# Optimization experiments

Measured on AMD Instinct MI355X. Metric: run time of the kernel, lower is better.

The kernel has to match this reference:

```python
import jax, jax.numpy as jnp
import numpy as np

EPS_GN = 1e-8
EPS_ATTN = 1e-8


def setup_inputs() -> dict:
    key = jax.random.key(0)
    ks = jax.random.split(key, 13)
    B, C, N = 4, 512, 2048
    s = 0.02
    return {
        "x": jax.random.normal(ks[0], (B, C, N), jnp.float32),
        "dw_w": jax.random.normal(ks[1], (C, 3), jnp.float32) * s,
        "pw_w": jax.random.normal(ks[2], (C, C), jnp.float32) * s,
        "u_w": jax.random.normal(ks[3], (2 * C, C), jnp.float32) * s,
        "u_b": jax.random.normal(ks[4], (2 * C,), jnp.float32) * s,
        "v_w": jax.random.normal(ks[5], (2 * C, C), jnp.float32) * s,
        "v_b": jax.random.normal(ks[6], (2 * C,), jnp.float32) * s,
        "h_w": jax.random.normal(ks[7], (C, C), jnp.float32) * s,
        "h_b": jax.random.normal(ks[8], (C,), jnp.float32) * s,
        "q_w": jax.random.normal(ks[9], (C, C), jnp.float32) * s,
        "k_w": jax.random.normal(ks[10], (C, C), jnp.float32) * s,
        "o_w": jax.random.normal(ks[11], (C, 2 * C), jnp.float32) * s,
        "o_b": jax.random.normal(ks[12], (C,), jnp.float32) * s,
    }


def reference(x, dw_w, pw_w, u_w, u_b, v_w, v_b, h_w, h_b, q_w, k_w, o_w, o_b):
    # x: [B, C, N]
    C = x.shape[1]
    # GroupNorm(1, C): normalize over (C, N) per sample; affine is identity-init
    # in torch but we follow the module math with default weight=1, bias=0
    mean = jnp.mean(x, axis=(1, 2), keepdims=True)
    var = jnp.var(x, axis=(1, 2), keepdims=True)
    z = (x - mean) * jax.lax.rsqrt(var + EPS_GN)

    # local depthwise conv k=3, pad=1 (cross-correlation), no bias
    zp = jnp.pad(z, ((0, 0), (0, 0), (1, 1)))
    dw = (dw_w[:, 0, None] * zp[:, :, :-2]
          + dw_w[:, 1, None] * zp[:, :, 1:-1]
          + dw_w[:, 2, None] * zp[:, :, 2:])
    # pointwise conv (no bias)
    z = z + jnp.einsum('oc,bcn->bon', pw_w, dw)

    u = jax.nn.sigmoid(jnp.einsum('oc,bcn->bon', u_w, z) + u_b[:, None])  # [B,2C,N]
    v = jnp.einsum('oc,bcn->bon', v_w, z) + v_b[:, None]                  # [B,2C,N]
    h = jnp.einsum('oc,bcn->bno', h_w, z) + h_b                           # [B,N,C]

    q = h @ q_w.T  # [B,N,C]
    k = h @ k_w.T  # [B,N,C]
    scale = 1.0 / jnp.sqrt(jnp.float32(C))

    logits = jnp.einsum('bnc,bmc->bnm', q, k) * scale
    a = jax.nn.relu(logits)
    a = a * a
    a = a / (jnp.sum(a, axis=-1, keepdims=True) + EPS_ATTN)

    av = jnp.einsum('bnm,bom->bon', a, v)  # [B,2C,N]
    y = jnp.einsum('oc,bcn->bon', o_w, u * av) + o_b[:, None]
    return x + y
```

## Files before the change

### kernel.cpp

```cpp
#include <hip/hip_runtime.h>
#include <hip/hip_bf16.h>
#include <cstdint>

typedef __bf16 bhalf;
typedef __bf16 bhalf8 __attribute__((ext_vector_type(8)));
typedef float f32x4 __attribute__((ext_vector_type(4)));

enum { EPI_Z2=0, EPI_BIAS=2, EPI_QK=3, EPI_Y=6, EPI_ST=7 };

__device__ __forceinline__ void gl_lds16(const void* g, void* l) {
  __builtin_amdgcn_global_load_lds(
      (const __attribute__((address_space(1))) unsigned int*)g,
      (__attribute__((address_space(3))) unsigned int*)l,
      16, 0, 0);
}
__device__ __forceinline__ void barrier_raw() { asm volatile("s_barrier" ::: "memory"); }
#define VMW(n)  asm volatile("s_waitcnt vmcnt(" #n ")" ::: "memory")
#define LGKM0() asm volatile("s_waitcnt lgkmcnt(0)" ::: "memory")

__device__ __forceinline__ unsigned char to_fp8(float v){
  return (unsigned char)(__builtin_amdgcn_cvt_pk_fp8_f32(v, v, 0, false) & 0xff);
}


__global__ void __launch_bounds__(256, 2)
gsc8(const unsigned char* __restrict__ Q, const unsigned char* __restrict__ Kp,
     unsigned char* __restrict__ Wsc, float* __restrict__ rden, float scale)
{
  constexpr int DBUF = 256*64;
  __shared__ __align__(16) char lds[3*DBUF];

  const int gx = gridDim.x, gy = gridDim.y;
  const int nwg = gx*gy;
  const int flat = blockIdx.y*gx + blockIdx.x;
  const int q8 = nwg>>3, r8 = nwg&7, xcd = flat&7, o8 = flat>>3;
  const int w = (xcd<r8 ? xcd*(q8+1) : r8*(q8+1)+(xcd-r8)*q8) + o8;
  const int bx = w % gx, by = w / gx;
  const int m0 = by*128, n0 = bx*128;
  const int bz = blockIdx.z;
  const int K = 512;

  const unsigned char* Ab = Q  + (long)bz*2048*512;
  const unsigned char* Bb = Kp + (long)bz*2048*512;

  const int tid = threadIdx.x;
  const int wid = tid>>6, lane = tid&63;
  const int lm = lane&15, kq = lane>>4;
  const int wm = wid>>1, wn = wid&1;
  const int srow = lane>>2;
  const int csw8 = ((lane&3) ^ ((lane>>3)&3))*16;
  int coff[2];
  #pragma unroll
  for (int ksl=0; ksl<2; ksl++)
    coff[ksl] = ((((ksl*2 + (kq>>1)) ^ ((lm>>1)&3)))<<4) + ((kq&1)<<3);

  f32x4 acc[4][4];
  #pragma unroll
  for (int i=0;i<4;i++)
    #pragma unroll
    for (int j=0;j<4;j++) acc[i][j] = f32x4{0.f,0.f,0.f,0.f};

  auto stage = [&](int kt){
    char* base = lds + (kt%3)*DBUF;
    const int k0 = kt*64;
    #pragma unroll
    for (int c=0;c<4;c++){
      const int r0 = c*64 + wid*16;
      char* d = base + r0*64;
      const unsigned char* g = (r0 < 128)
        ? Ab + (long)(m0 + r0 + srow)*K + k0 + csw8
        : Bb + (long)(n0 + r0 - 128 + srow)*K + k0 + csw8;
      gl_lds16(g, d);
    }
  };

  long af[4][2], bf[4][2];
  auto readA = [&](int kt){
    char* base = lds + (kt%3)*DBUF;
    #pragma unroll
    for (int i2=0;i2<4;i2++)
      #pragma unroll
      for (int ksl=0;ksl<2;ksl++)
        af[i2][ksl] = *(const long*)(base + (wm*64 + i2*16 + lm)*64 + coff[ksl]);
  };
  auto readB = [&](int kt, int jh){
    char* base = lds + (kt%3)*DBUF;
    #pragma unroll
    for (int j2=0;j2<2;j2++)
      #pragma unroll
      for (int ksl=0;ksl<2;ksl++)
        bf[jh*2+j2][ksl] = *(const long*)(base + (128 + wn*64 + jh*32 + j2*16 + lm)*64 + coff[ksl]);
  };
  auto mfma16 = [&](int jh){
    __builtin_amdgcn_s_setprio(1);
    #pragma unroll
    for (int i2=0;i2<4;i2++)
      #pragma unroll
      for (int j2=0;j2<2;j2++)
        #pragma unroll
        for (int ksl=0;ksl<2;ksl++)
          acc[i2][jh*2+j2] = __builtin_amdgcn_mfma_f32_16x16x32_fp8_fp8(
              af[i2][ksl], bf[jh*2+j2][ksl], acc[i2][jh*2+j2], 0,0,0);
    __builtin_amdgcn_s_setprio(0);
  };

  const int NT = 8;
  stage(0); stage(1);
  for (int kt=0; kt<NT; ++kt){
    if (kt==NT-1) { VMW(0); } else { VMW(4); }
    barrier_raw();
    readA(kt); readB(kt,0);
    if (kt+2<NT) stage(kt+2);
    mfma16(0);
    readB(kt,1);
    mfma16(1);
  }
  barrier_raw();

  float rs[4][4];
  #pragma unroll
  for (int i=0;i<4;i++)
    #pragma unroll
    for (int r=0;r<4;r++) rs[i][r]=0.f;
  #pragma unroll
  for (int i=0;i<4;i++){
    #pragma unroll
    for (int j=0;j<4;j++){
      const int lcol = wn*64 + j*16 + lm;
      #pragma unroll
      for (int r=0;r<4;r++){
        const int lrow = wm*64 + i*16 + kq*4 + r;
        float v = acc[i][j][r];
        v *= scale; v = fmaxf(v,0.f); v = v*v;
        rs[i][r] += v;
        const int lb = lrow*128 + ((((lcol>>4) ^ (lrow&7)))<<4) + (lcol&15);
        *(unsigned char*)(lds + lb) = to_fp8(v);
      }
    }
  }
  float* rd = rden + (long)bz*2048;
  #pragma unroll
  for (int i=0;i<4;i++){
    const int rbase = m0 + wm*64 + i*16 + kq*4;
    #pragma unroll
    for (int r=0;r<4;r++){
      float s = rs[i][r];
      s += __shfl_xor(s,1); s += __shfl_xor(s,2);
      s += __shfl_xor(s,4); s += __shfl_xor(s,8);
      if (lm==0) atomicAdd(rd + rbase + r, s);
    }
  }
  LGKM0();
  barrier_raw();
  unsigned char* obase = Wsc + (long)bz*2048*2048 + (long)m0*2048 + n0;
  #pragma unroll
  for (int it=0; it<4; ++it){
    const int g = (it*256 + tid)*16;
    const int row = g >> 7, off = g & 127;
    const int lb = row*128 + ((((off>>4) ^ (row&7)))<<4);
    uint4 val = *(const uint4*)(lds + lb);
    *(uint4*)(obase + (long)row*2048 + off) = val;
  }
}

__global__ void __launch_bounds__(256, 2)
guv8(const unsigned char* __restrict__ A, const unsigned char* __restrict__ Bw,
     bhalf* __restrict__ Ub, unsigned char* __restrict__ Vfm,
     const float* __restrict__ ubias, const float* __restrict__ vbias)
{
  constexpr int DBUF = 256*64;
  __shared__ __align__(16) char lds[3*DBUF];

  const int gx = gridDim.x, gy = gridDim.y;
  const int nwg = gx*gy;
  const int flat = blockIdx.y*gx + blockIdx.x;
  const int q8 = nwg>>3, r8 = nwg&7, xcd = flat&7, o8 = flat>>3;
  const int w = (xcd<r8 ? xcd*(q8+1) : r8*(q8+1)+(xcd-r8)*q8) + o8;
  const int bx = w % gx, by = w / gx;
  const int m0 = by*128, n0 = bx*128;
  const int K = 512;

  const int tid = threadIdx.x;
  const int wid = tid>>6, lane = tid&63;
  const int lm = lane&15, kq = lane>>4;
  const int wm = wid>>1, wn = wid&1;
  const int srow = lane>>2;
  const int csw8 = ((lane&3) ^ ((lane>>3)&3))*16;
  int coff[2];
  #pragma unroll
  for (int ksl=0; ksl<2; ksl++)
    coff[ksl] = ((((ksl*2 + (kq>>1)) ^ ((lm>>1)&3)))<<4) + ((kq&1)<<3);

  f32x4 acc[4][4];
  #pragma unroll
  for (int i=0;i<4;i++)
    #pragma unroll
    for (int j=0;j<4;j++) acc[i][j] = f32x4{0.f,0.f,0.f,0.f};

  auto stage = [&](int kt){
    char* base = lds + (kt%3)*DBUF;
    const int k0 = kt*64;
    #pragma unroll
    for (int c=0;c<4;c++){
      const int r0 = c*64 + wid*16;
      char* d = base + r0*64;
      const unsigned char* g = (r0 < 128)
        ? A  + (long)(m0 + r0 + srow)*K + k0 + csw8
        : Bw + (long)(n0 + r0 - 128 + srow)*K + k0 + csw8;
      gl_lds16(g, d);
    }
  };

  long af[4][2], bf[4][2];
  auto readA = [&](int kt){
    char* base = lds + (kt%3)*DBUF;
    #pragma unroll
    for (int i2=0;i2<4;i2++)
      #pragma unroll
      for (int ksl=0;ksl<2;ksl++)
        af[i2][ksl] = *(const long*)(base + (wm*64 + i2*16 + lm)*64 + coff[ksl]);
  };
  auto readB = [&](int kt, int jh){
    char* base = lds + (kt%3)*DBUF;
    #pragma unroll
    for (int j2=0;j2<2;j2++)
      #pragma unroll
      for (int ksl=0;ksl<2;ksl++)
        bf[jh*2+j2][ksl] = *(const long*)(base + (128 + wn*64 + jh*32 + j2*16 + lm)*64 + coff[ksl]);
  };
  auto mfma16 = [&](int jh){
    __builtin_amdgcn_s_setprio(1);
    #pragma unroll
    for (int i2=0;i2<4;i2++)
      #pragma unroll
      for (int j2=0;j2<2;j2++)
        #pragma unroll
        for (int ksl=0;ksl<2;ksl++)
          acc[i2][jh*2+j2] = __builtin_amdgcn_mfma_f32_16x16x32_fp8_fp8(
              af[i2][ksl], bf[jh*2+j2][ksl], acc[i2][jh*2+j2], 0,0,0);
    __builtin_amdgcn_s_setprio(0);
  };

  const int NT = 8;
  stage(0); stage(1);
  for (int kt=0; kt<NT; ++kt){
    if (kt==NT-1) { VMW(0); } else { VMW(4); }
    barrier_raw();
    readA(kt); readB(kt,0);
    if (kt+2<NT) stage(kt+2);
    mfma16(0);
    readB(kt,1);
    mfma16(1);
  }
  barrier_raw();

  const bool uh = n0 < 1024;
  if (uh){
    #pragma unroll
    for (int i=0;i<4;i++){
      #pragma unroll
      for (int j=0;j<4;j++){
        const int lcol = wn*64 + j*16 + lm;
        #pragma unroll
        for (int r=0;r<4;r++){
          const int lrow = wm*64 + i*16 + kq*4 + r;
          float v = acc[i][j][r] + ubias[n0 + lcol];
          v = 1.f/(1.f + __expf(-v));
          const int cb = lcol*2;
          const int lb = lrow*256 + (((cb>>5) ^ ((lrow>>2)&3))<<5) + (cb&31);
          *(bhalf*)(lds + lb) = (bhalf)v;
        }
      }
    }
    LGKM0();
    barrier_raw();
    char* obase = (char*)Ub + 2*((long)m0*1024 + n0);
    #pragma unroll
    for (int it=0; it<8; ++it){
      const int g = (it*256 + tid)*16;
      const int row = g >> 8, off = g & 255;
      const int lb = row*256 + (((off>>5) ^ ((row>>2)&3))<<5) + (off&31);
      uint4 val = *(const uint4*)(lds + lb);
      *(uint4*)(obase + (long)row*2048 + off) = val;
    }
  } else {
    #pragma unroll
    for (int i=0;i<4;i++){
      #pragma unroll
      for (int j=0;j<4;j++){
        const int lcol = wn*64 + j*16 + lm;
        #pragma unroll
        for (int r=0;r<4;r++){
          const int lrow = wm*64 + i*16 + kq*4 + r;
          float v = acc[i][j][r] + vbias[n0 - 1024 + lcol];
          const int lb = lcol*128 + ((((lrow>>4) ^ (lcol&7)))<<4) + (lrow&15);
          *(unsigned char*)(lds + lb) = to_fp8(v);
        }
      }
    }
    LGKM0();
    barrier_raw();
    unsigned char* vb = Vfm + ((long)(m0>>11)*1024*2048 + (long)(n0-1024)*2048 + (m0 & 2047));
    #pragma unroll
    for (int it=0; it<4; ++it){
      const int g = (it*256 + tid)*16;
      const int row = g >> 7, off = g & 127;
      const int lb = row*128 + ((((off>>4) ^ (row&7)))<<4);
      uint4 val = *(const uint4*)(lds + lb);
      *(uint4*)(vb + (long)row*2048 + off) = val;
    }
  }
}

__global__ void __launch_bounds__(256, 2)
g4k8(const unsigned char* __restrict__ A, const unsigned char* __restrict__ Bw,
     bhalf* __restrict__ Out,
     const bhalf* __restrict__ ub, const float* __restrict__ rden,
     int K, long sB, int rowshift)
{
  constexpr int DBUF = 256*64;
  __shared__ __align__(16) char lds[4*DBUF];

  const int gx = gridDim.x, gy = gridDim.y;
  const int nwg = gx*gy;
  const int flat = blockIdx.y*gx + blockIdx.x;
  const int q8 = nwg>>3, r8 = nwg&7, xcd = flat&7, o8 = flat>>3;
  const int w = (xcd<r8 ? xcd*(q8+1) : r8*(q8+1)+(xcd-r8)*q8) + o8;
  const int bx = w % gx, by = w / gx;
  const int m0 = by*128, n0 = bx*128;

  const unsigned char* Bb = Bw + (long)(m0>>rowshift)*sB;

  const int tid = threadIdx.x;
  const int wid = tid>>6, lane = tid&63;
  const int lm = lane&15, kq = lane>>4;
  const int wm = wid>>1, wn = wid&1;
  const int srow = lane>>2;
  const int csw8 = ((lane&3) ^ ((lane>>3)&3))*16;
  int coff[2];
  #pragma unroll
  for (int ksl=0; ksl<2; ksl++)
    coff[ksl] = ((((ksl*2 + (kq>>1)) ^ ((lm>>1)&3)))<<4) + ((kq&1)<<3);

  f32x4 acc[4][4];
  #pragma unroll
  for (int i=0;i<4;i++)
    #pragma unroll
    for (int j=0;j<4;j++) acc[i][j] = f32x4{0.f,0.f,0.f,0.f};

  auto stage = [&](int kt){
    char* base = lds + (kt&3)*DBUF;
    const int k0 = kt*64;
    #pragma unroll
    for (int c=0;c<4;c++){
      const int r0 = c*64 + wid*16;
      char* d = base + r0*64;
      const unsigned char* g = (r0 < 128)
        ? A  + (long)(m0 + r0 + srow)*K + k0 + csw8
        : Bb + (long)(n0 + r0 - 128 + srow)*K + k0 + csw8;
      gl_lds16(g, d);
    }
  };

  long af[4][2], bf[4][2];
  auto readA = [&](int kt){
    char* base = lds + (kt&3)*DBUF;
    #pragma unroll
    for (int i2=0;i2<4;i2++)
      #pragma unroll
      for (int ksl=0;ksl<2;ksl++)
        af[i2][ksl] = *(const long*)(base + (wm*64 + i2*16 + lm)*64 + coff[ksl]);
  };
  auto readB = [&](int kt, int jh){
    char* base = lds + (kt&3)*DBUF;
    #pragma unroll
    for (int j2=0;j2<2;j2++)
      #pragma unroll
      for (int ksl=0;ksl<2;ksl++)
        bf[jh*2+j2][ksl] = *(const long*)(base + (128 + wn*64 + jh*32 + j2*16 + lm)*64 + coff[ksl]);
  };
  auto mfma16 = [&](int jh){
    __builtin_amdgcn_s_setprio(1);
    #pragma unroll
    for (int i2=0;i2<4;i2++)
      #pragma unroll
      for (int j2=0;j2<2;j2++)
        #pragma unroll
        for (int ksl=0;ksl<2;ksl++)
          acc[i2][jh*2+j2] = __builtin_amdgcn_mfma_f32_16x16x32_fp8_fp8(
              af[i2][ksl], bf[jh*2+j2][ksl], acc[i2][jh*2+j2], 0,0,0);
    __builtin_amdgcn_s_setprio(0);
  };

  const int NT = K>>6;
  stage(0); stage(1); stage(2);
  for (int kt=0; kt<NT; ++kt){
    if (kt==NT-1)      { VMW(0); }
    else if (kt==NT-2) { VMW(4); }
    else               { VMW(8); }
    barrier_raw();
    readA(kt); readB(kt,0);
    if (kt+3<NT) stage(kt+3);
    mfma16(0);
    readB(kt,1);
    mfma16(1);
  }
  barrier_raw();

  char* obase = (char*)Out + 2*((long)m0*1024 + n0);
  #pragma unroll
  for (int i=0;i<4;i++){
    #pragma unroll
    for (int j=0;j<4;j++){
      const int lcol = wn*64 + j*16 + lm;
      #pragma unroll
      for (int r=0;r<4;r++){
        const int lrow = wm*64 + i*16 + kq*4 + r;
        const int rowg = m0 + lrow;
        float v = acc[i][j][r];
        float den = rden[rowg];
        v *= __builtin_amdgcn_rcpf(den + 1e-8f);
        v *= (float)ub[(long)rowg*1024 + n0 + lcol];
        const int cb = lcol*2;
        const int lb = lrow*256 + (((cb>>5) ^ ((lrow>>2)&3))<<5) + (cb&31);
        *(bhalf*)(lds + lb) = (bhalf)v;
      }
    }
  }
  LGKM0();
  barrier_raw();
  #pragma unroll
  for (int it=0; it<8; ++it){
    const int g = (it*256 + tid)*16;
    const int row = g >> 8, off = g & 255;
    const int lb = row*256 + (((off>>5) ^ ((row>>2)&3))<<5) + (off&31);
    uint4 val = *(const uint4*)(lds + lb);
    *(uint4*)(obase + (long)row*2048 + off) = val;
  }
}

template<int EPI>
__global__ void __launch_bounds__(256, 2)
g4k(const bhalf* __restrict__ A, const bhalf* __restrict__ Bw,
    void* __restrict__ Out, void* __restrict__ Out2,
    const float* __restrict__ bias,
    const bhalf* __restrict__ auxb,
    const float* __restrict__ xadd,
    int M, int N, int K)
{
  constexpr int KSL = 256*64;
  constexpr int DBUF = 2*KSL;
  __shared__ __align__(16) char lds[2*DBUF];

  const int gx = gridDim.x, gy = gridDim.y;
  const int nwg = gx*gy;
  const int flat = blockIdx.y*gx + blockIdx.x;
  const int q8 = nwg>>3, r8 = nwg&7, xcd = flat&7, o8 = flat>>3;
  const int w = (xcd<r8 ? xcd*(q8+1) : r8*(q8+1)+(xcd-r8)*q8) + o8;
  const int bx = w % gx, by = w / gx;
  const int m0 = by*128, n0 = bx*128;

  const int tid = threadIdx.x;
  const int wid = tid>>6, lane = tid&63;
  const int lm = lane&15, kq = lane>>4;
  const int wm = wid>>1, wn = wid&1;
  const int srow = lane>>2;
  const int csw = ((lane&3) ^ ((lane>>3)&3))*8;
  const int kqs = kq ^ ((lm>>1)&3);

  f32x4 acc[4][4];
  #pragma unroll
  for (int i=0;i<4;i++)
    #pragma unroll
    for (int j=0;j<4;j++) acc[i][j] = f32x4{0.f,0.f,0.f,0.f};

  auto stage = [&](int kt){
    char* base = lds + (kt&1)*DBUF;
    const int k0 = kt*64;
    #pragma unroll
    for (int c=0;c<4;c++){
      const int r0 = c*64 + wid*16;
      #pragma unroll
      for (int ksl=0; ksl<2; ksl++){
        bhalf* d = (bhalf*)(base + ksl*KSL + r0*64);
        const bhalf* g = (r0 < 128)
          ? A  + (long)(m0 + r0 + srow)*K + k0 + ksl*32 + csw
          : Bw + (long)(n0 + r0 - 128 + srow)*K + k0 + ksl*32 + csw;
        gl_lds16(g, d);
      }
    }
  };

  bhalf8 af[4][2], bf[4][2];
  auto readA = [&](int kt){
    char* base = lds + (kt&1)*DBUF;
    #pragma unroll
    for (int i2=0;i2<4;i2++)
      #pragma unroll
      for (int ksl=0;ksl<2;ksl++)
        af[i2][ksl] = *(const bhalf8*)(base + ksl*KSL + (wm*64 + i2*16 + lm)*64 + kqs*16);
  };
  auto readB = [&](int kt, int jh){
    char* base = lds + (kt&1)*DBUF;
    #pragma unroll
    for (int j2=0;j2<2;j2++)
      #pragma unroll
      for (int ksl=0;ksl<2;ksl++)
        bf[jh*2+j2][ksl] = *(const bhalf8*)(base + ksl*KSL + (128 + wn*64 + jh*32 + j2*16 + lm)*64 + kqs*16);
  };
  auto mfma16 = [&](int jh){
    __builtin_amdgcn_s_setprio(1);
    #pragma unroll
    for (int i2=0;i2<4;i2++)
      #pragma unroll
      for (int j2=0;j2<2;j2++)
        #pragma unroll
        for (int ksl=0;ksl<2;ksl++)
          acc[i2][jh*2+j2] = __builtin_amdgcn_mfma_f32_16x16x32_bf16(
              af[i2][ksl], bf[jh*2+j2][ksl], acc[i2][jh*2+j2], 0,0,0);
    __builtin_amdgcn_s_setprio(0);
  };

  const int NT = K>>6;
  stage(0); stage(1);
  for (int kt=0; kt<NT; ++kt){
    if (kt==NT-1) { VMW(0); } else { VMW(8); }
    barrier_raw();
    readA(kt); readB(kt,0);
    mfma16(0);
    barrier_raw();
    readB(kt,1);
    if (kt+2<NT) stage(kt+2);
    mfma16(1);
  }
  barrier_raw();

  if constexpr (EPI==EPI_Y){
    #pragma unroll
    for (int i=0;i<4;i++){
      #pragma unroll
      for (int j=0;j<4;j++){
        const int lcol = wn*64 + j*16 + lm;
        #pragma unroll
        for (int r=0;r<4;r++){
          const int lrow = wm*64 + i*16 + kq*4 + r;
          float v = acc[i][j][r] + bias[n0 + lcol];
          const int lb = lcol*512 + 4*(lrow ^ ((lcol&15)<<2));
          *(float*)(lds + lb) = v;
        }
      }
    }
    LGKM0();
    barrier_raw();
    const int b = m0 >> 11, nb = m0 & 2047;
    float* ob = (float*)Out + ((long)b*512 + n0)*2048 + nb;
    const float* xb = xadd + ((long)b*512 + n0)*2048 + nb;
    #pragma unroll
    for (int it=0; it<16; ++it){
      const int g = (it*256 + tid)*16;
      const int row = g >> 9, off = g & 511;
      const int t0 = off >> 2;
      const int s = (row&15)<<2;
      f32x4 vv = *(const f32x4*)(lds + row*512 + 4*(t0^s));
      f32x4 xx = *(const f32x4*)(xb + (long)row*2048 + t0);
      *(f32x4*)(ob + (long)row*2048 + t0) = vv + xx;
    }
  } else if constexpr (EPI==EPI_QK){
    bool qh = n0 < 512;
    unsigned char* obase = (unsigned char*)(qh?Out:Out2) + (long)m0*512 + (n0 - (qh?0:512));
    #pragma unroll
    for (int i=0;i<4;i++){
      #pragma unroll
      for (int j=0;j<4;j++){
        const int lcol = wn*64 + j*16 + lm;
        #pragma unroll
        for (int r=0;r<4;r++){
          const int lrow = wm*64 + i*16 + kq*4 + r;
          float v = acc[i][j][r] + bias[n0 + lcol];
          const int lb = lrow*128 + ((((lcol>>4) ^ (lrow&7)))<<4) + (lcol&15);
          *(unsigned char*)(lds + lb) = to_fp8(v);
        }
      }
    }
    LGKM0();
    barrier_raw();
    #pragma unroll
    for (int it=0; it<4; ++it){
      const int g = (it*256 + tid)*16;
      const int row = g >> 7, off = g & 127;
      const int lb = row*128 + ((((off>>4) ^ (row&7)))<<4);
      uint4 val = *(const uint4*)(lds + lb);
      *(uint4*)(obase + (long)row*512 + off) = val;
    }
  } else {
    char* obase = (char*)Out + 2*((long)m0*N + n0);
    const int ldb = N*2;
    #pragma unroll
    for (int i=0;i<4;i++){
      #pragma unroll
      for (int j=0;j<4;j++){
        const int lcol = wn*64 + j*16 + lm;
        #pragma unroll
        for (int r=0;r<4;r++){
          const int lrow = wm*64 + i*16 + kq*4 + r;
          float v = acc[i][j][r];
          if constexpr (EPI==EPI_Z2)
            v += (float)auxb[(long)(m0+lrow)*N + n0 + lcol];
          if constexpr (EPI==EPI_BIAS)
            v += bias[n0 + lcol];
          const int cb = lcol*2;
          const int lb = lrow*256 + (((cb>>5) ^ ((lrow>>2)&3))<<5) + (cb&31);
          *(bhalf*)(lds + lb) = (bhalf)v;
          if constexpr (EPI==EPI_Z2){
            const int lb2 = 32768 + lrow*128 + ((((lcol>>4) ^ (lrow&7)))<<4) + (lcol&15);
            *(unsigned char*)(lds + lb2) = to_fp8(v);
          }
        }
      }
    }
    LGKM0();
    barrier_raw();
    #pragma unroll
    for (int it=0; it<8; ++it){
      const int g = (it*256 + tid)*16;
      const int row = g >> 8, off = g & 255;
      const int lb = row*256 + (((off>>5) ^ ((row>>2)&3))<<5) + (off&31);
      uint4 val = *(const uint4*)(lds + lb);
      *(uint4*)(obase + (long)row*ldb + off) = val;
    }
    if constexpr (EPI==EPI_Z2){
      unsigned char* o8 = (unsigned char*)Out2 + (long)m0*N + n0;
      #pragma unroll
      for (int it=0; it<4; ++it){
        const int g = (it*256 + tid)*16;
        const int row = g >> 7, off = g & 127;
        const int lb = 32768 + row*128 + ((((off>>4) ^ (row&7)))<<4);
        uint4 val = *(const uint4*)(lds + lb);
        *(uint4*)(o8 + (long)row*N + off) = val;
      }
    }
  }
  (void)M; (void)xadd; (void)bias; (void)auxb;
}

struct CvtArgs { const float* src[5]; bhalf* dst[5]; int n[5]; };
__global__ void cvt_multi(CvtArgs a) {
  int seg = blockIdx.y;
  int i = (blockIdx.x*256 + threadIdx.x)*4;
  if (i >= a.n[seg]) return;
  float4 f = *(const float4*)(a.src[seg] + i);
  bhalf* d = a.dst[seg] + i;
  d[0]=(bhalf)f.x; d[1]=(bhalf)f.y; d[2]=(bhalf)f.z; d[3]=(bhalf)f.w;
}

__global__ void cvt_fp8(const float* __restrict__ src, unsigned char* __restrict__ dst, int n){
  int i = (blockIdx.x*256 + threadIdx.x)*4;
  if (i >= n) return;
  float4 f = *(const float4*)(src + i);
  dst[i+0]=to_fp8(f.x); dst[i+1]=to_fp8(f.y);
  dst[i+2]=to_fp8(f.z); dst[i+3]=to_fp8(f.w);
}

__global__ void transpose_bf16(const bhalf* __restrict__ in, bhalf* __restrict__ out,
                               int R, int C) {
  __shared__ bhalf t[32][33];
  int r0 = blockIdx.x*32, c0 = blockIdx.y*32;
  int tx = threadIdx.x, ty = threadIdx.y;
  #pragma unroll
  for (int r=0;r<4;r++)
    t[ty + r*8][tx] = in[(long)(r0 + ty + r*8)*C + c0 + tx];
  __syncthreads();
  #pragma unroll
  for (int r=0;r<4;r++)
    out[(long)(c0 + ty + r*8)*R + r0 + tx] = t[tx][ty + r*8];
}

__global__ void qk_bias(const bhalf* __restrict__ wqk, const float* __restrict__ hb,
                        float* __restrict__ bq){
  int row = blockIdx.x*4 + (threadIdx.x>>6);
  int lane = threadIdx.x & 63;
  const bhalf* p = wqk + (long)row*512;
  float s = 0.f;
  #pragma unroll
  for (int j=0;j<8;j++) s += (float)p[lane*8+j] * hb[lane*8+j];
  for (int off=32; off; off>>=1) s += __shfl_xor(s, off);
  if (lane==0) bq[row] = s;
}

__global__ void gn_part(const float* __restrict__ x, float* __restrict__ ps, float* __restrict__ pss) {
  int b = blockIdx.y;
  const float* xb = x + (long)b*(512*2048);
  float s=0.f, ss=0.f;
  #pragma unroll
  for (int it=0; it<8; it++){
    int idx = ((it*128 + blockIdx.x)*256 + threadIdx.x)*4;
    float4 f = *(const float4*)(xb + idx);
    s  += f.x+f.y+f.z+f.w;
    ss += f.x*f.x+f.y*f.y+f.z*f.z+f.w*f.w;
  }
  for (int off=32; off; off>>=1){ s += __shfl_xor(s,off); ss += __shfl_xor(ss,off); }
  __shared__ float ls[4], lss[4];
  int wid = threadIdx.x>>6, lane = threadIdx.x&63;
  if (lane==0){ ls[wid]=s; lss[wid]=ss; }
  __syncthreads();
  if (threadIdx.x==0){
    s = ls[0]+ls[1]+ls[2]+ls[3]; ss = lss[0]+lss[1]+lss[2]+lss[3];
    ps[b*128 + blockIdx.x] = s; pss[b*128 + blockIdx.x] = ss;
  }
}

__global__ void gn_final(const float* __restrict__ ps, const float* __restrict__ pss,
                         float* __restrict__ stats) {
  int b = blockIdx.x;
  float s = ps[b*128 + threadIdx.x], ss = pss[b*128 + threadIdx.x];
  for (int off=32; off; off>>=1){ s += __shfl_xor(s,off); ss += __shfl_xor(ss,off); }
  __shared__ float l0[2], l1[2];
  int wid = threadIdx.x>>6, lane = threadIdx.x&63;
  if (lane==0){ l0[wid]=s; l1[wid]=ss; }
  __syncthreads();
  if (threadIdx.x==0){
    s = l0[0]+l0[1]; ss = l1[0]+l1[1];
    float mean = s*(1.f/1048576.f);
    float var  = ss*(1.f/1048576.f) - mean*mean;
    stats[b*2] = mean; stats[b*2+1] = rsqrtf(var + 1e-8f);
  }
}

__global__ void norm_dw_T(const float* __restrict__ x, const float* __restrict__ stats,
                          const float* __restrict__ dw_w,
                          bhalf* __restrict__ zT, bhalf* __restrict__ dwT) {
  int b = blockIdx.z, n0 = blockIdx.x*32, c0 = blockIdx.y*32;
  float mean = stats[b*2], rstd = stats[b*2+1];
  __shared__ float zs[32][35];
  int tx = threadIdx.x, ty = threadIdx.y;
  #pragma unroll
  for (int r=0;r<4;r++){
    int c = c0 + ty + r*8;
    for (int cc=tx; cc<34; cc+=32){
      int n = n0 - 1 + cc;
      float v = 0.f;
      if (n>=0 && n<2048) v = (x[((long)b*512 + c)*2048 + n] - mean)*rstd;
      zs[ty + r*8][cc] = v;
    }
  }
  __syncthreads();
  float w0 = dw_w[(c0+tx)*3+0], w1 = dw_w[(c0+tx)*3+1], w2 = dw_w[(c0+tx)*3+2];
  #pragma unroll
  for (int r=0;r<4;r++){
    int ln = ty + r*8;
    float z = zs[tx][ln+1];
    float d = w0*zs[tx][ln] + w1*zs[tx][ln+1] + w2*zs[tx][ln+2];
    long o = ((long)b*2048 + n0 + ln)*512 + c0 + tx;
    zT[o] = (bhalf)z; dwT[o] = (bhalf)d;
  }
}

extern "C" void kernel_launch(void* const* d_in, const int* in_sizes, int n_in,
                              void* d_out, int out_size, void* d_ws, size_t ws_size,
                              hipStream_t stream) {
  (void)in_sizes; (void)n_in; (void)out_size; (void)ws_size;
  const float* x    = (const float*)d_in[0];
  const float* dw_w = (const float*)d_in[1];
  const float* pw_w = (const float*)d_in[2];
  const float* u_w  = (const float*)d_in[3];
  const float* u_b  = (const float*)d_in[4];
  const float* v_w  = (const float*)d_in[5];
  const float* v_b  = (const float*)d_in[6];
  const float* h_w  = (const float*)d_in[7];
  const float* h_b  = (const float*)d_in[8];
  const float* q_w  = (const float*)d_in[9];
  const float* k_w  = (const float*)d_in[10];
  const float* o_w  = (const float*)d_in[11];
  const float* o_b  = (const float*)d_in[12];
  float* out = (float*)d_out;

  char* ws = (char*)d_ws;
  size_t off = 0;
  auto alloc = [&](size_t bytes) -> void* {
    void* p = ws + off; off = (off + bytes + 255) & ~(size_t)255; return p;
  };

  float* ps    = (float*)alloc(4*128*4);
  float* pss   = (float*)alloc(4*128*4);
  float* stats = (float*)alloc(4*2*4);
  float* rden  = (float*)alloc(4*2048*4);
  float* bq    = (float*)alloc(1024*4);
  bhalf* wb_pw = (bhalf*)alloc(512*512*2);
  unsigned char* wuv8 = (unsigned char*)alloc((size_t)2048*512);
  bhalf* wb_h  = (bhalf*)alloc(512*512*2);
  bhalf* hwT   = (bhalf*)alloc(512*512*2);
  bhalf* wb_qk = (bhalf*)alloc((size_t)1024*512*2);
  bhalf* wqk2  = (bhalf*)alloc((size_t)1024*512*2);
  bhalf* wb_o  = (bhalf*)alloc((size_t)512*1024*2);
  const size_t ACT = (size_t)4*2048*512;
  bhalf* zT   = (bhalf*)alloc(ACT*2);
  bhalf* dwT  = (bhalf*)alloc(ACT*2);
  bhalf* z2T  = (bhalf*)alloc(ACT*2);
  unsigned char* z2f8 = (unsigned char*)alloc(ACT);
  bhalf* ub   = (bhalf*)alloc(ACT*2*2);
  unsigned char* v_fm = (unsigned char*)alloc((size_t)4*1024*2048);
  unsigned char* wsc  = (unsigned char*)alloc((size_t)4*2048*2048);
  unsigned char* qb8  = (unsigned char*)alloc(ACT);
  unsigned char* kb8  = (unsigned char*)alloc(ACT);
  bhalf* uav  = (bhalf*)alloc(ACT*2*2);

  hipMemsetAsync(rden, 0, 4*2048*4, stream);

  CvtArgs ca;
  ca.src[0]=pw_w; ca.dst[0]=wb_pw;           ca.n[0]=512*512;
  ca.src[1]=h_w;  ca.dst[1]=wb_h;            ca.n[1]=512*512;
  ca.src[2]=q_w;  ca.dst[2]=wb_qk;           ca.n[2]=512*512;
  ca.src[3]=k_w;  ca.dst[3]=wb_qk+512*512;   ca.n[3]=512*512;
  ca.src[4]=o_w;  ca.dst[4]=wb_o;            ca.n[4]=512*1024;
  cvt_multi<<<dim3(512,5), 256, 0, stream>>>(ca);
  cvt_fp8<<<dim3(512), 256, 0, stream>>>(u_w, wuv8,          1024*512);
  cvt_fp8<<<dim3(512), 256, 0, stream>>>(v_w, wuv8+1024*512, 1024*512);

  transpose_bf16<<<dim3(16,16), dim3(32,8), 0, stream>>>(wb_h, hwT, 512, 512);
  g4k<EPI_ST><<<dim3(4,8,1), 256, 0, stream>>>(wb_qk, hwT, wqk2, nullptr,
      nullptr, nullptr, nullptr, 1024, 512, 512);
  qk_bias<<<dim3(256), 256, 0, stream>>>(wb_qk, h_b, bq);

  gn_part<<<dim3(128,4), 256, 0, stream>>>(x, ps, pss);
  gn_final<<<dim3(4), 128, 0, stream>>>(ps, pss, stats);

  norm_dw_T<<<dim3(64,16,4), dim3(32,8), 0, stream>>>(x, stats, dw_w, zT, dwT);

  const float iscl = 0.044194173824159216f;
  g4k<EPI_Z2><<<dim3(4,64,1), 256, 0, stream>>>(dwT, wb_pw, z2T, z2f8,
      nullptr, zT, nullptr, 8192, 512, 512);
  guv8<<<dim3(16,64,1), 256, 0, stream>>>(z2f8, wuv8, ub, v_fm, u_b, v_b);
  g4k<EPI_QK><<<dim3(8,64,1), 256, 0, stream>>>(z2T, wqk2, qb8, kb8,
      bq, nullptr, nullptr, 8192, 1024, 512);
  gsc8<<<dim3(16,16,4), 256, 0, stream>>>(qb8, kb8, wsc, rden, iscl);
  g4k8<<<dim3(8,64,1), 256, 0, stream>>>(wsc, v_fm, uav, ub, rden,
      2048, (long)1024*2048, 11);
  g4k<EPI_Y><<<dim3(4,64,1), 256, 0, stream>>>(uav, wb_o, out, nullptr,
      o_b, nullptr, x, 8192, 512, 1024);
}
```

Before: 172.8 us.

## Convert QK projection and output projection GEMMs to FP8 with scaled weights

Result: no change. 171.1 us (-1.0%).

```diff
diff --git a/kernel.cpp b/kernel.cpp
--- a/kernel.cpp
+++ b/kernel.cpp
@@ -6,7 +6,7 @@
 typedef __bf16 bhalf8 __attribute__((ext_vector_type(8)));
 typedef float f32x4 __attribute__((ext_vector_type(4)));
 
-enum { EPI_Z2=0, EPI_BIAS=2, EPI_QK=3, EPI_Y=6, EPI_ST=7 };
+enum { EPI_Z2=0, EPI_ST=7 };
 
 __device__ __forceinline__ void gl_lds16(const void* g, void* l) {
   __builtin_amdgcn_global_load_lds(
@@ -313,8 +313,127 @@
 }
 
 __global__ void __launch_bounds__(256, 2)
+gqk8(const unsigned char* __restrict__ A, const unsigned char* __restrict__ Bw,
+     unsigned char* __restrict__ Qo, unsigned char* __restrict__ Ko,
+     const float* __restrict__ bq)
+{
+  constexpr int DBUF = 256*64;
+  __shared__ __align__(16) char lds[3*DBUF];
+
+  const int gx = gridDim.x, gy = gridDim.y;
+  const int nwg = gx*gy;
+  const int flat = blockIdx.y*gx + blockIdx.x;
+  const int q8 = nwg>>3, r8 = nwg&7, xcd = flat&7, o8 = flat>>3;
+  const int w = (xcd<r8 ? xcd*(q8+1) : r8*(q8+1)+(xcd-r8)*q8) + o8;
+  const int bx = w % gx, by = w / gx;
+  const int m0 = by*128, n0 = bx*128;
+  const int K = 512;
+
+  const int tid = threadIdx.x;
+  const int wid = tid>>6, lane = tid&63;
+  const int lm = lane&15, kq = lane>>4;
+  const int wm = wid>>1, wn = wid&1;
+  const int srow = lane>>2;
+  const int csw8 = ((lane&3) ^ ((lane>>3)&3))*16;
+  int coff[2];
+  #pragma unroll
+  for (int ksl=0; ksl<2; ksl++)
+    coff[ksl] = ((((ksl*2 + (kq>>1)) ^ ((lm>>1)&3)))<<4) + ((kq&1)<<3);
+
+  f32x4 acc[4][4];
+  #pragma unroll
+  for (int i=0;i<4;i++)
+    #pragma unroll
+    for (int j=0;j<4;j++) acc[i][j] = f32x4{0.f,0.f,0.f,0.f};
+
+  auto stage = [&](int kt){
+    char* base = lds + (kt%3)*DBUF;
+    const int k0 = kt*64;
+    #pragma unroll
+    for (int c=0;c<4;c++){
+      const int r0 = c*64 + wid*16;
+      char* d = base + r0*64;
+      const unsigned char* g = (r0 < 128)
+        ? A  + (long)(m0 + r0 + srow)*K + k0 + csw8
+        : Bw + (long)(n0 + r0 - 128 + srow)*K + k0 + csw8;
+      gl_lds16(g, d);
+    }
+  };
+
+  long af[4][2], bf[4][2];
+  auto readA = [&](int kt){
+    char* base = lds + (kt%3)*DBUF;
+    #pragma unroll
+    for (int i2=0;i2<4;i2++)
+      #pragma unroll
+      for (int ksl=0;ksl<2;ksl++)
+        af[i2][ksl] = *(const long*)(base + (wm*64 + i2*16 + lm)*64 + coff[ksl]);
+  };
+  auto readB = [&](int kt, int jh){
+    char* base = lds + (kt%3)*DBUF;
+    #pragma unroll
+    for (int j2=0;j2<2;j2++)
+      #pragma unroll
+      for (int ksl=0;ksl<2;ksl++)
+        bf[jh*2+j2][ksl] = *(const long*)(base + (128 + wn*64 + jh*32 + j2*16 + lm)*64 + coff[ksl]);
+  };
+  auto mfma16 = [&](int jh){
+    __builtin_amdgcn_s_setprio(1);
+    #pragma unroll
+    for (int i2=0;i2<4;i2++)
+      #pragma unroll
+      for (int j2=0;j2<2;j2++)
+        #pragma unroll
+        for (int ksl=0;ksl<2;ksl++)
+          acc[i2][jh*2+j2] = __builtin_amdgcn_mfma_f32_16x16x32_fp8_fp8(
+              af[i2][ksl], bf[jh*2+j2][ksl], acc[i2][jh*2+j2], 0,0,0);
+    __builtin_amdgcn_s_setprio(0);
+  };
+
+  const int NT = 8;
+  stage(0); stage(1);
+  for (int kt=0; kt<NT; ++kt){
+    if (kt==NT-1) { VMW(0); } else { VMW(4); }
+    barrier_raw();
+    readA(kt); readB(kt,0);
+    if (kt+2<NT) stage(kt+2);
+    mfma16(0);
+    readB(kt,1);
+    mfma16(1);
+  }
+  barrier_raw();
+
+  bool qh = n0 < 512;
+  unsigned char* obase = (qh?Qo:Ko) + (long)m0*512 + (n0 - (qh?0:512));
+  #pragma unroll
+  for (int i=0;i<4;i++){
+    #pragma unroll
+    for (int j=0;j<4;j++){
+      const int lcol = wn*64 + j*16 + lm;
+      #pragma unroll
+      for (int r=0;r<4;r++){
+        const int lrow = wm*64 + i*16 + kq*4 + r;
+        float v = acc[i][j][r] + 16.f*bq[n0 + lcol];
+        const int lb = lrow*128 + ((((lcol>>4) ^ (lrow&7)))<<4) + (lcol&15);
+        *(unsigned char*)(lds + lb) = to_fp8(v);
+      }
+    }
+  }
+  LGKM0();
+  barrier_raw();
+  #pragma unroll
+  for (int it=0; it<4; ++it){
+    const int g = (it*256 + tid)*16;
+    const int row = g >> 7, off = g & 127;
+    const int lb = row*128 + ((((off>>4) ^ (row&7)))<<4);
+    uint4 val = *(const uint4*)(lds + lb);
+    *(uint4*)(obase + (long)row*512 + off) = val;
+  }
+}
+
+__global__ void __launch_bounds__(256, 2)
 g4k8(const unsigned char* __restrict__ A, const unsigned char* __restrict__ Bw,
-     bhalf* __restrict__ Out,
+     unsigned char* __restrict__ Out,
      const bhalf* __restrict__ ub, const float* __restrict__ rden,
      int K, long sB, int rowshift)
 {
@@ -407,7 +526,7 @@
   }
   barrier_raw();
 
-  char* obase = (char*)Out + 2*((long)m0*1024 + n0);
+  unsigned char* obase = Out + (long)m0*1024 + n0;
   #pragma unroll
   for (int i=0;i<4;i++){
     #pragma unroll
@@ -421,31 +540,152 @@
         float den = rden[rowg];
         v *= __builtin_amdgcn_rcpf(den + 1e-8f);
         v *= (float)ub[(long)rowg*1024 + n0 + lcol];
-        const int cb = lcol*2;
-        const int lb = lrow*256 + (((cb>>5) ^ ((lrow>>2)&3))<<5) + (cb&31);
-        *(bhalf*)(lds + lb) = (bhalf)v;
+        const int lb = lrow*128 + ((((lcol>>4) ^ (lrow&7)))<<4) + (lcol&15);
+        *(unsigned char*)(lds + lb) = to_fp8(v);
       }
     }
   }
   LGKM0();
   barrier_raw();
   #pragma unroll
-  for (int it=0; it<8; ++it){
+  for (int it=0; it<4; ++it){
     const int g = (it*256 + tid)*16;
-    const int row = g >> 8, off = g & 255;
-    const int lb = row*256 + (((off>>5) ^ ((row>>2)&3))<<5) + (off&31);
+    const int row = g >> 7, off = g & 127;
+    const int lb = row*128 + ((((off>>4) ^ (row&7)))<<4);
     uint4 val = *(const uint4*)(lds + lb);
-    *(uint4*)(obase + (long)row*2048 + off) = val;
+    *(uint4*)(obase + (long)row*1024 + off) = val;
+  }
+}
+
+__global__ void __launch_bounds__(256, 2)
+gy8(const unsigned char* __restrict__ A, const unsigned char* __restrict__ Bw,
+    float* __restrict__ Out, const float* __restrict__ bias,
+    const float* __restrict__ xadd)
+{
+  constexpr int DBUF = 256*64;
+  __shared__ __align__(16) char lds[4*DBUF];
+
+  const int gx = gridDim.x, gy = gridDim.y;
+  const int nwg = gx*gy;
+  const int flat = blockIdx.y*gx + blockIdx.x;
+  const int q8 = nwg>>3, r8 = nwg&7, xcd = flat&7, o8 = flat>>3;
+  const int w = (xcd<r8 ? xcd*(q8+1) : r8*(q8+1)+(xcd-r8)*q8) + o8;
+  const int bx = w % gx, by = w / gx;
+  const int m0 = by*128, n0 = bx*128;
+  const int K = 1024;
+
+  const int tid = threadIdx.x;
+  const int wid = tid>>6, lane = tid&63;
+  const int lm = lane&15, kq = lane>>4;
+  const int wm = wid>>1, wn = wid&1;
+  const int srow = lane>>2;
+  const int csw8 = ((lane&3) ^ ((lane>>3)&3))*16;
+  int coff[2];
+  #pragma unroll
+  for (int ksl=0; ksl<2; ksl++)
+    coff[ksl] = ((((ksl*2 + (kq>>1)) ^ ((lm>>1)&3)))<<4) + ((kq&1)<<3);
+
+  f32x4 acc[4][4];
+  #pragma unroll
+  for (int i=0;i<4;i++)
+    #pragma unroll
+    for (int j=0;j<4;j++) acc[i][j] = f32x4{0.f,0.f,0.f,0.f};
+
+  auto stage = [&](int kt){
+    char* base = lds + (kt&3)*DBUF;
+    const int k0 = kt*64;
+    #pragma unroll
+    for (int c=0;c<4;c++){
+      const int r0 = c*64 + wid*16;
+      char* d = base + r0*64;
+      const unsigned char* g = (r0 < 128)
+        ? A  + (long)(m0 + r0 + srow)*K + k0 + csw8
+        : Bw + (long)(n0 + r0 - 128 + srow)*K + k0 + csw8;
+      gl_lds16(g, d);
+    }
+  };
+
+  long af[4][2], bf[4][2];
+  auto readA = [&](int kt){
+    char* base = lds + (kt&3)*DBUF;
+    #pragma unroll
+    for (int i2=0;i2<4;i2++)
+      #pragma unroll
+      for (int ksl=0;ksl<2;ksl++)
+        af[i2][ksl] = *(const long*)(base + (wm*64 + i2*16 + lm)*64 + coff[ksl]);
+  };
+  auto readB = [&](int kt, int jh){
+    char* base = lds + (kt&3)*DBUF;
+    #pragma unroll
+    for (int j2=0;j2<2;j2++)
+      #pragma unroll
+      for (int ksl=0;ksl<2;ksl++)
+        bf[jh*2+j2][ksl] = *(const long*)(base + (128 + wn*64 + jh*32 + j2*16 + lm)*64 + coff[ksl]);
+  };
+  auto mfma16 = [&](int jh){
+    __builtin_amdgcn_s_setprio(1);
+    #pragma unroll
+    for (int i2=0;i2<4;i2++)
+      #pragma unroll
+      for (int j2=0;j2<2;j2++)
+        #pragma unroll
+        for (int ksl=0;ksl<2;ksl++)
+          acc[i2][jh*2+j2] = __builtin_amdgcn_mfma_f32_16x16x32_fp8_fp8(
+              af[i2][ksl], bf[jh*2+j2][ksl], acc[i2][jh*2+j2], 0,0,0);
+    __builtin_amdgcn_s_setprio(0);
+  };
+
+  const int NT = 16;
+  stage(0); stage(1); stage(2);
+  for (int kt=0; kt<NT; ++kt){
+    if (kt==NT-1)      { VMW(0); }
+    else if (kt==NT-2) { VMW(4); }
+    else               { VMW(8); }
+    barrier_raw();
+    readA(kt); readB(kt,0);
+    if (kt+3<NT) stage(kt+3);
+    mfma16(0);
+    readB(kt,1);
+    mfma16(1);
+  }
+  barrier_raw();
+
+  #pragma unroll
+  for (int i=0;i<4;i++){
+    #pragma unroll
+    for (int j=0;j<4;j++){
+      const int lcol = wn*64 + j*16 + lm;
+      #pragma unroll
+      for (int r=0;r<4;r++){
+        const int lrow = wm*64 + i*16 + kq*4 + r;
+        float v = acc[i][j][r]*0.0625f + bias[n0 + lcol];
+        const int lb = lcol*512 + 4*(lrow ^ ((lcol&15)<<2));
+        *(float*)(lds + lb) = v;
+      }
+    }
+  }
+  LGKM0();
+  barrier_raw();
+  const int b = m0 >> 11, nb = m0 & 2047;
+  float* ob = Out + ((long)b*512 + n0)*2048 + nb;
+  const float* xb = xadd + ((long)b*512 + n0)*2048 + nb;
+  #pragma unroll
+  for (int it=0; it<16; ++it){
+    const int g = (it*256 + tid)*16;
+    const int row = g >> 9, off = g & 511;
+    const int t0 = off >> 2;
+    const int s = (row&15)<<2;
+    f32x4 vv = *(const f32x4*)(lds + row*512 + 4*(t0^s));
+    f32x4 xx = *(const f32x4*)(xb + (long)row*2048 + t0);
+    *(f32x4*)(ob + (long)row*2048 + t0) = vv + xx;
   }
 }
 
 template<int EPI>
 __global__ void __launch_bounds__(256, 2)
 g4k(const bhalf* __restrict__ A, const bhalf* __restrict__ Bw,
-    void* __restrict__ Out, void* __restrict__ Out2,
-    const float* __restrict__ bias,
+    void* __restrict__ Out,
     const bhalf* __restrict__ auxb,
-    const float* __restrict__ xadd,
     int M, int N, int K)
 {
   constexpr int KSL = 256*64;
@@ -535,7 +775,8 @@
   }
   barrier_raw();
 
-  if constexpr (EPI==EPI_Y){
+  if constexpr (EPI==EPI_Z2){
+    unsigned char* obase = (unsigned char*)Out + (long)m0*N + n0;
     #pragma unroll
     for (int i=0;i<4;i++){
       #pragma unroll
@@ -544,30 +785,25 @@
         #pragma unroll
         for (int r=0;r<4;r++){
           const int lrow = wm*64 + i*16 + kq*4 + r;
-          float v = acc[i][j][r] + bias[n0 + lcol];
-          const int lb = lcol*512 + 4*(lrow ^ ((lcol&15)<<2));
-          *(float*)(lds + lb) = v;
+          float v = acc[i][j][r] + (float)auxb[(long)(m0+lrow)*N + n0 + lcol];
+          const int lb = lrow*128 + ((((lcol>>4) ^ (lrow&7)))<<4) + (lcol&15);
+          *(unsigned char*)(lds + lb) = to_fp8(v);
         }
       }
     }
     LGKM0();
     barrier_raw();
-    const int b = m0 >> 11, nb = m0 & 2047;
-    float* ob = (float*)Out + ((long)b*512 + n0)*2048 + nb;
-    const float* xb = xadd + ((long)b*512 + n0)*2048 + nb;
-    #pragma unroll
-    for (int it=0; it<16; ++it){
+    #pragma unroll
+    for (int it=0; it<4; ++it){
       const int g = (it*256 + tid)*16;
-      const int row = g >> 9, off = g & 511;
-      const int t0 = off >> 2;
-      const int s = (row&15)<<2;
-      f32x4 vv = *(const f32x4*)(lds + row*512 + 4*(t0^s));
-      f32x4 xx = *(const f32x4*)(xb + (long)row*2048 + t0);
-      *(f32x4*)(ob + (long)row*2048 + t0) = vv + xx;
-    }
-  } else if constexpr (EPI==EPI_QK){
-    bool qh = n0 < 512;
-    unsigned char* obase = (unsigned char*)(qh?Out:Out2) + (long)m0*512 + (n0 - (qh?0:512));
+      const int row = g >> 7, off = g & 127;
+      const int lb = row*128 + ((((off>>4) ^ (row&7)))<<4);
+      uint4 val = *(const uint4*)(lds + lb);
+      *(uint4*)(obase + (long)row*N + off) = val;
+    }
+  } else {
+    char* obase = (char*)Out + 2*((long)m0*N + n0);
+    const int ldb = N*2;
     #pragma unroll
     for (int i=0;i<4;i++){
       #pragma unroll
@@ -576,45 +812,9 @@
         #pragma unroll
         for (int r=0;r<4;r++){
           const int lrow = wm*64 + i*16 + kq*4 + r;
-          float v = acc[i][j][r] + bias[n0 + lcol];
-          const int lb = lrow*128 + ((((lcol>>4) ^ (lrow&7)))<<4) + (lcol&15);
-          *(unsigned char*)(lds + lb) = to_fp8(v);
-        }
-      }
-    }
-    LGKM0();
-    barrier_raw();
-    #pragma unroll
-    for (int it=0; it<4; ++it){
-      const int g = (it*256 + tid)*16;
-      const int row = g >> 7, off = g & 127;
-      const int lb = row*128 + ((((off>>4) ^ (row&7)))<<4);
-      uint4 val = *(const uint4*)(lds + lb);
-      *(uint4*)(obase + (long)row*512 + off) = val;
-    }
-  } else {
-    char* obase = (char*)Out + 2*((long)m0*N + n0);
-    const int ldb = N*2;
-    #pragma unroll
-    for (int i=0;i<4;i++){
-      #pragma unroll
-      for (int j=0;j<4;j++){
-        const int lcol = wn*64 + j*16 + lm;
-        #pragma unroll
-        for (int r=0;r<4;r++){
-          const int lrow = wm*64 + i*16 + kq*4 + r;
-          float v = acc[i][j][r];
-          if constexpr (EPI==EPI_Z2)
-            v += (float)auxb[(long)(m0+lrow)*N + n0 + lcol];
-          if constexpr (EPI==EPI_BIAS)
-            v += bias[n0 + lcol];
           const int cb = lcol*2;
           const int lb = lrow*256 + (((cb>>5) ^ ((lrow>>2)&3))<<5) + (cb&31);
-          *(bhalf*)(lds + lb) = (bhalf)v;
-          if constexpr (EPI==EPI_Z2){
-            const int lb2 = 32768 + lrow*128 + ((((lcol>>4) ^ (lrow&7)))<<4) + (lcol&15);
-            *(unsigned char*)(lds + lb2) = to_fp8(v);
-          }
+          *(bhalf*)(lds + lb) = (bhalf)acc[i][j][r];
         }
       }
     }
@@ -628,22 +828,11 @@
       uint4 val = *(const uint4*)(lds + lb);
       *(uint4*)(obase + (long)row*ldb + off) = val;
     }
-    if constexpr (EPI==EPI_Z2){
-      unsigned char* o8 = (unsigned char*)Out2 + (long)m0*N + n0;
-      #pragma unroll
-      for (int it=0; it<4; ++it){
-        const int g = (it*256 + tid)*16;
-        const int row = g >> 7, off = g & 127;
-        const int lb = 32768 + row*128 + ((((off>>4) ^ (row&7)))<<4);
-        uint4 val = *(const uint4*)(lds + lb);
-        *(uint4*)(o8 + (long)row*N + off) = val;
-      }
-    }
-  }
-  (void)M; (void)xadd; (void)bias; (void)auxb;
-}
-
-struct CvtArgs { const float* src[5]; bhalf* dst[5]; int n[5]; };
+  }
+  (void)M; (void)auxb;
+}
+
+struct CvtArgs { const float* src[4]; bhalf* dst[4]; int n[4]; };
 __global__ void cvt_multi(CvtArgs a) {
   int seg = blockIdx.y;
   int i = (blockIdx.x*256 + threadIdx.x)*4;
@@ -653,12 +842,21 @@
   d[0]=(bhalf)f.x; d[1]=(bhalf)f.y; d[2]=(bhalf)f.z; d[3]=(bhalf)f.w;
 }
 
-__global__ void cvt_fp8(const float* __restrict__ src, unsigned char* __restrict__ dst, int n){
+__global__ void cvt_fp8(const float* __restrict__ src, unsigned char* __restrict__ dst,
+                        int n, float scale){
   int i = (blockIdx.x*256 + threadIdx.x)*4;
   if (i >= n) return;
   float4 f = *(const float4*)(src + i);
-  dst[i+0]=to_fp8(f.x); dst[i+1]=to_fp8(f.y);
-  dst[i+2]=to_fp8(f.z); dst[i+3]=to_fp8(f.w);
+  dst[i+0]=to_fp8(f.x*scale); dst[i+1]=to_fp8(f.y*scale);
+  dst[i+2]=to_fp8(f.z*scale); dst[i+3]=to_fp8(f.w*scale);
+}
+
+__global__ void cvt_b2f8(const bhalf* __restrict__ src, unsigned char* __restrict__ dst,
+                         int n, float scale){
+  int i = (blockIdx.x*256 + threadIdx.x)*4;
+  if (i >= n) return;
+  #pragma unroll
+  for (int j=0;j<4;j++) dst[i+j] = to_fp8((float)src[i+j]*scale);
 }
 
 __global__ void transpose_bf16(const bhalf* __restrict__ in, bhalf* __restrict__ out,
@@ -786,23 +984,23 @@
   float* rden  = (float*)alloc(4*2048*4);
   float* bq    = (float*)alloc(1024*4);
   bhalf* wb_pw = (bhalf*)alloc(512*512*2);
-  unsigned char* wuv8 = (unsigned char*)alloc((size_t)2048*512);
+  unsigned char* wuv8  = (unsigned char*)alloc((size_t)2048*512);
+  unsigned char* wo8   = (unsigned char*)alloc((size_t)512*1024);
   bhalf* wb_h  = (bhalf*)alloc(512*512*2);
   bhalf* hwT   = (bhalf*)alloc(512*512*2);
   bhalf* wb_qk = (bhalf*)alloc((size_t)1024*512*2);
   bhalf* wqk2  = (bhalf*)alloc((size_t)1024*512*2);
-  bhalf* wb_o  = (bhalf*)alloc((size_t)512*1024*2);
+  unsigned char* wqk28 = (unsigned char*)alloc((size_t)1024*512);
   const size_t ACT = (size_t)4*2048*512;
   bhalf* zT   = (bhalf*)alloc(ACT*2);
   bhalf* dwT  = (bhalf*)alloc(ACT*2);
-  bhalf* z2T  = (bhalf*)alloc(ACT*2);
   unsigned char* z2f8 = (unsigned char*)alloc(ACT);
   bhalf* ub   = (bhalf*)alloc(ACT*2*2);
   unsigned char* v_fm = (unsigned char*)alloc((size_t)4*1024*2048);
   unsigned char* wsc  = (unsigned char*)alloc((size_t)4*2048*2048);
   unsigned char* qb8  = (unsigned char*)alloc(ACT);
   unsigned char* kb8  = (unsigned char*)alloc(ACT);
-  bhalf* uav  = (bhalf*)alloc(ACT*2*2);
+  unsigned char* uav8 = (unsigned char*)alloc(ACT*2);
 
   hipMemsetAsync(rden, 0, 4*2048*4, stream);
 
@@ -811,30 +1009,29 @@
   ca.src[1]=h_w;  ca.dst[1]=wb_h;            ca.n[1]=512*512;
   ca.src[2]=q_w;  ca.dst[2]=wb_qk;           ca.n[2]=512*512;
   ca.src[3]=k_w;  ca.dst[3]=wb_qk+512*512;   ca.n[3]=512*512;
-  ca.src[4]=o_w;  ca.dst[4]=wb_o;            ca.n[4]=512*1024;
-  cvt_multi<<<dim3(512,5), 256, 0, stream>>>(ca);
-  cvt_fp8<<<dim3(512), 256, 0, stream>>>(u_w, wuv8,          1024*512);
-  cvt_fp8<<<dim3(512), 256, 0, stream>>>(v_w, wuv8+1024*512, 1024*512);
+  cvt_multi<<<dim3(512,4), 256, 0, stream>>>(ca);
+  cvt_fp8<<<dim3(512), 256, 0, stream>>>(u_w, wuv8,          1024*512, 1.f);
+  cvt_fp8<<<dim3(512), 256, 0, stream>>>(v_w, wuv8+1024*512, 1024*512, 1.f);
+  cvt_fp8<<<dim3(512), 256, 0, stream>>>(o_w, wo8,           512*1024, 16.f);
 
   transpose_bf16<<<dim3(16,16), dim3(32,8), 0, stream>>>(wb_h, hwT, 512, 512);
   g4k<EPI_ST><<<dim3(4,8,1), 256, 0, stream>>>(wb_qk, hwT, wqk2, nullptr,
-      nullptr, nullptr, nullptr, 1024, 512, 512);
+      1024, 512, 512);
   qk_bias<<<dim3(256), 256, 0, stream>>>(wb_qk, h_b, bq);
+  cvt_b2f8<<<dim3(512), 256, 0, stream>>>(wqk2, wqk28, 1024*512, 16.f);
 
   gn_part<<<dim3(128,4), 256, 0, stream>>>(x, ps, pss);
   gn_final<<<dim3(4), 128, 0, stream>>>(ps, pss, stats);
 
   norm_dw_T<<<dim3(64,16,4), dim3(32,8), 0, stream>>>(x, stats, dw_w, zT, dwT);
 
-  const float iscl = 0.044194173824159216f;
-  g4k<EPI_Z2><<<dim3(4,64,1), 256, 0, stream>>>(dwT, wb_pw, z2T, z2f8,
-      nullptr, zT, nullptr, 8192, 512, 512);
+  const float iscl256 = 0.044194173824159216f / 256.f;
+  g4k<EPI_Z2><<<dim3(4,64,1), 256, 0, stream>>>(dwT, wb_pw, z2f8, zT,
+      8192, 512, 512);
   guv8<<<dim3(16,64,1), 256, 0, stream>>>(z2f8, wuv8, ub, v_fm, u_b, v_b);
-  g4k<EPI_QK><<<dim3(8,64,1), 256, 0, stream>>>(z2T, wqk2, qb8, kb8,
-      bq, nullptr, nullptr, 8192, 1024, 512);
-  gsc8<<<dim3(16,16,4), 256, 0, stream>>>(qb8, kb8, wsc, rden, iscl);
-  g4k8<<<dim3(8,64,1), 256, 0, stream>>>(wsc, v_fm, uav, ub, rden,
+  gqk8<<<dim3(8,64,1), 256, 0, stream>>>(z2f8, wqk28, qb8, kb8, bq);
+  gsc8<<<dim3(16,16,4), 256, 0, stream>>>(qb8, kb8, wsc, rden, iscl256);
+  g4k8<<<dim3(8,64,1), 256, 0, stream>>>(wsc, v_fm, uav8, ub, rden,
       2048, (long)1024*2048, 11);
-  g4k<EPI_Y><<<dim3(4,64,1), 256, 0, stream>>>(uav, wb_o, out, nullptr,
-      o_b, nullptr, x, 8192, 512, 1024);
-}
+  gy8<<<dim3(4,64,1), 256, 0, stream>>>(uav8, wo8, out, o_b, x);
+}
```
